# Performance work log

Hardware: AMD Instinct MI355X
Metric: run time of the kernel (lower is better)

The kernel has to match this reference:

```python
import jax, jax.numpy as jnp
import numpy as np

B, S, H, MID = 8, 2048, 256, 32


def get_rotary_matrix(s, d):
    # Faithful to llama-from-scratch get_rotary_matrix: theta = 10000**(-2*(i-1)/d)
    pos = jnp.arange(s, dtype=jnp.float32)
    i = jnp.arange(d // 2, dtype=jnp.float32)
    theta = 10000.0 ** (-2.0 * (i - 1.0) / d)
    ang = pos[:, None] * theta[None, :]            # [s, d/2]
    c, sn = jnp.cos(ang), jnp.sin(ang)
    ev = 2 * jnp.arange(d // 2)
    od = ev + 1
    R = jnp.zeros((s, d, d), jnp.float32)
    R = R.at[:, ev, ev].set(c).at[:, od, od].set(c)
    R = R.at[:, ev, od].set(-sn).at[:, od, ev].set(sn)
    return R


def setup_inputs() -> dict:
    key = jax.random.key(0)
    ks = jax.random.split(key, 7)
    sc = 0.02
    x = jax.random.normal(ks[0], (B, S, H), jnp.float32)
    # nn.Linear weights: l1.weight [mid, in], l2.weight [out, mid]; y = x @ W.T
    wq1 = jax.random.normal(ks[1], (MID, H), jnp.float32) * sc
    wq2 = jax.random.normal(ks[2], (H, MID), jnp.float32) * sc
    wk1 = jax.random.normal(ks[3], (MID, H), jnp.float32) * sc
    wk2 = jax.random.normal(ks[4], (H, MID), jnp.float32) * sc
    wv1 = jax.random.normal(ks[5], (MID, H), jnp.float32) * sc
    wv2 = jax.random.normal(ks[6], (H, MID), jnp.float32) * sc
    r = get_rotary_matrix(S, H)                    # [S, H, H] buffer
    return {"x": x, "r": r, "wq1": wq1, "wq2": wq2, "wk1": wk1,
            "wk2": wk2, "wv1": wv1, "wv2": wv2}


def reference(x, r, wq1, wq2, wk1, wk2, wv1, wv2):
    b, s, h = x.shape
    q = (x @ wq1.T) @ wq2.T                        # LoRA q: [b,s,h]
    k = (x @ wk1.T) @ wk2.T
    v = (x @ wv1.T) @ wv2.T
    # RoPE as dense per-position rotation matmul (bmm over seq dim)
    qr = jnp.einsum('bsh,shk->bsk', q, r[:s])
    kr = jnp.einsum('bsh,shk->bsk', k, r[:s])
    attn = jnp.einsum('bqh,bkh->bqk', qr, kr) * (h ** -0.5)   # [b,s,s]
    mask = jnp.tril(jnp.ones((s, s), bool))
    attn = jnp.where(mask, attn, -jnp.inf)
    attn = jax.nn.softmax(attn, axis=-1)
    out = attn @ v                                 # [b,s,h]
    return out
```

## Files before the change

kernel.cpp:

```cpp
#include <hip/hip_runtime.h>
#include <hip/hip_bf16.h>
#include <math.h>

typedef float f32x4 __attribute__((ext_vector_type(4)));
typedef float f32x16 __attribute__((ext_vector_type(16)));
typedef unsigned int u32x4 __attribute__((ext_vector_type(4)));
typedef __bf16 bf16x8 __attribute__((ext_vector_type(8)));
typedef unsigned short u16;

#define MFMA16(acc, a, b)                                              \
  acc = __builtin_amdgcn_mfma_f32_16x16x32_bf16(                       \
      __builtin_bit_cast(bf16x8, a), __builtin_bit_cast(bf16x8, b),    \
      acc, 0, 0, 0)

#define MFMA32(acc, a, b)                                              \
  acc = __builtin_amdgcn_mfma_f32_32x32x16_bf16(                       \
      __builtin_bit_cast(bf16x8, a), __builtin_bit_cast(bf16x8, b),    \
      acc, 0, 0, 0)

#define GLOAD_LDS16(gp, lp)                                            \
  __builtin_amdgcn_global_load_lds(                                    \
      (const __attribute__((address_space(1))) void*)(const void*)(gp),\
      (__attribute__((address_space(3))) void*)(void*)(lp), 16, 0, 0)

__device__ __forceinline__ u16 f2bf(float f) {
  union { float f; unsigned u; } v; v.f = f;
  unsigned r = v.u + 0x7FFFu + ((v.u >> 16) & 1u);
  return (u16)(r >> 16);
}

__device__ __forceinline__ float b2f(u16 h) {
  union { unsigned u; float f; } v; v.u = ((unsigned)h) << 16; return v.f;
}

__device__ __forceinline__ unsigned cvtpk(float lo, float hi) {
  unsigned r;
  asm("v_cvt_pk_bf16_f32 %0, %1, %2" : "=v"(r) : "v"(lo), "v"(hi));
  return r;
}

#define BFEX(vec, e) ((u16)(((e) & 1) ? ((vec)[(e) >> 1] >> 16) : ((vec)[(e) >> 1] & 0xffffu)))

__global__ __launch_bounds__(256) void proj_kernel(
    const float* __restrict__ x,
    const float* __restrict__ w1q, const float* __restrict__ w2q,
    const float* __restrict__ w1k, const float* __restrict__ w2k,
    const float* __restrict__ w1v, const float* __restrict__ w2v,
    u16* __restrict__ qout, u16* __restrict__ kout, u16* __restrict__ vout)
{
  __shared__ __align__(16) u16 smem[37376];
  u16* xs  = smem;
  u16* w1s = smem + 16384;
  u16* w2s = smem + 24576;
  u16* tls = smem + 34816;
  u16* bnc = smem;

  const int tid = threadIdx.x;
  const int w = tid >> 6, l = tid & 63;
  const int l15 = l & 15, lg = l >> 4;
  const int row0 = blockIdx.x * 64;
  const int p = blockIdx.y;

  const float* w1 = (p == 0) ? w1q : (p == 1) ? w1k : w1v;
  const float* w2 = (p == 0) ? w2q : (p == 1) ? w2k : w2v;
  u16* outp = (p == 0) ? qout : (p == 1) ? kout : vout;
  const bool dorope = (p < 2);

  #pragma unroll
  for (int i = 0; i < 16; ++i) {
    int idx = tid + 256 * i;
    int r = idx >> 6, c4 = idx & 63;
    float4 v = reinterpret_cast<const float4*>(x)[(size_t)(row0 + r) * 64 + c4];
    int ci = (c4 * 4) ^ ((r & 7) << 3);
    *reinterpret_cast<ushort4*>(&xs[r * 256 + ci]) =
        make_ushort4(f2bf(v.x), f2bf(v.y), f2bf(v.z), f2bf(v.w));
  }
  #pragma unroll
  for (int i = 0; i < 8; ++i) {
    int idx = tid + 256 * i;
    int r = idx >> 6, c4 = idx & 63;
    float4 v = reinterpret_cast<const float4*>(w1)[idx];
    int ci = (c4 * 4) ^ ((r & 7) << 3);
    *reinterpret_cast<ushort4*>(&w1s[r * 256 + ci]) =
        make_ushort4(f2bf(v.x), f2bf(v.y), f2bf(v.z), f2bf(v.w));
  }
  #pragma unroll
  for (int i = 0; i < 8; ++i) {
    int idx = tid + 256 * i;
    int r = idx >> 3, c4 = idx & 7;
    float4 v = reinterpret_cast<const float4*>(w2)[idx];
    *reinterpret_cast<ushort4*>(&w2s[r * 40 + c4 * 4]) =
        make_ushort4(f2bf(v.x), f2bf(v.y), f2bf(v.z), f2bf(v.w));
  }
  __syncthreads();

  f32x4 acc0 = {0.f, 0.f, 0.f, 0.f}, acc1 = {0.f, 0.f, 0.f, 0.f};
  {
    const int arow = w * 16 + l15;
    #pragma unroll
    for (int kk = 0; kk < 8; ++kk) {
      u32x4 a = *reinterpret_cast<const u32x4*>(
          &xs[arow * 256 + ((kk * 32 + lg * 8) ^ ((arow & 7) << 3))]);
      const int b0r = l15, b1r = l15 + 16;
      u32x4 b0 = *reinterpret_cast<const u32x4*>(
          &w1s[b0r * 256 + ((kk * 32 + lg * 8) ^ ((b0r & 7) << 3))]);
      u32x4 b1 = *reinterpret_cast<const u32x4*>(
          &w1s[b1r * 256 + ((kk * 32 + lg * 8) ^ ((b1r & 7) << 3))]);
      MFMA16(acc0, a, b0);
      MFMA16(acc1, a, b1);
    }
  }
  #pragma unroll
  for (int rr = 0; rr < 4; ++rr) {
    int trow = w * 16 + lg * 4 + rr;
    tls[trow * 40 + l15]      = f2bf(acc0[rr]);
    tls[trow * 40 + 16 + l15] = f2bf(acc1[rr]);
  }

  f32x4 yac[16];
  #pragma unroll
  for (int oc = 0; oc < 16; ++oc) yac[oc] = (f32x4){0.f, 0.f, 0.f, 0.f};
  {
    u32x4 a = *reinterpret_cast<const u32x4*>(&tls[(w * 16 + l15) * 40 + lg * 8]);
    #pragma unroll
    for (int oc = 0; oc < 16; ++oc) {
      u32x4 b = *reinterpret_cast<const u32x4*>(&w2s[(oc * 16 + l15) * 40 + lg * 8]);
      MFMA16(yac[oc], a, b);
    }
  }
  __syncthreads();

  #pragma unroll
  for (int oc = 0; oc < 16; ++oc)
    #pragma unroll
    for (int rr = 0; rr < 4; ++rr)
      bnc[(w * 16 + lg * 4 + rr) * 264 + oc * 16 + l15] = f2bf(yac[oc][rr]);
  __syncthreads();

  {
    const int frow = tid >> 2, c0 = (tid & 3) * 64;
    const int grow = row0 + frow;
    const int sidx = grow & 2047;
    const float sfl = (float)sidx;
    #pragma unroll
    for (int seg = 0; seg < 8; ++seg) {
      u32x4 v8 = *reinterpret_cast<const u32x4*>(&bnc[frow * 264 + c0 + seg * 8]);
      u32x4 res = v8;
      if (dorope) {
        #pragma unroll
        for (int j = 0; j < 4; ++j) {
          int jp = (c0 >> 1) + seg * 4 + j;
          float theta = __builtin_exp2f(13.287712379549449f *
                                        (2.f - 2.f * (float)jp) * (1.f / 256.f));
          float ang = sfl * theta;
          float sn, c;
          sincosf(ang, &sn, &c);
          float ev = b2f(BFEX(v8, 2 * j)), od = b2f(BFEX(v8, 2 * j + 1));
          u16 re = f2bf(ev * c + od * sn);
          u16 ro = f2bf(od * c - ev * sn);
          res[j] = ((unsigned)ro << 16) | (unsigned)re;
        }
      }
      *reinterpret_cast<u32x4*>(&outp[(size_t)grow * 256 + c0 + seg * 8]) = res;
    }
  }
}

__global__ __launch_bounds__(256, 2) void attn_kernel(
    const u16* __restrict__ qg, const u16* __restrict__ kg,
    const u16* __restrict__ vg, u16* __restrict__ po,
    float* __restrict__ pmw, float* __restrict__ plw)
{
  __shared__ __align__(16) u16 ks2[2][32 * 256];
  __shared__ __align__(16) u16 vt2[2][256 * 40];
  __shared__ float paxw[4][32];

  const int tid = threadIdx.x;
  const int w = tid >> 6, l = tid & 63;
  const int s = w >> 1, h2 = w & 1;
  const int q31 = l & 31, g = l >> 5;

  const int bx = blockIdx.x;
  const int bb = bx & 7;
  const int o_ = bx >> 3;
  const int idx = (o_ < 32) ? o_ : 95 - o_;
  const int qt = 31 - (idx >> 1);
  const int hv = idx & 1;
  const int tmx = 2 * qt + 1;

  const int qbase = qt * 64;
  const size_t boff = (size_t)bb * (2048 * 256);
  const int qg_ = qbase + s * 32 + q31;

  u32x4 qf[16];
  {
    const u16* qp = qg + boff + (size_t)qg_ * 256 + g * 8;
    #pragma unroll
    for (int st = 0; st < 16; ++st)
      qf[st] = *reinterpret_cast<const u32x4*>(qp + st * 16);
  }

  f32x16 o[4];
  #pragma unroll
  for (int dt = 0; dt < 4; ++dt)
    #pragma unroll
    for (int r = 0; r < 16; ++r) o[dt][r] = 0.f;
  float m_run = -INFINITY, l_run = 0.f;

  const int vc = tid & 31;
  const int kvr = (tid >> 5) * 4;
  const int swv = (vc & 3) << 3;
  const int swr = (q31 >> 3) << 3;
  const int ksw = (q31 & 7) << 3;
  const int kbase = q31 * 256;

  const u16* kgb = kg + boff;
  const u16* vgb = vg + boff;

  {
    const u16* kp = kgb + (size_t)(hv * 32) * 256;
    #pragma unroll
    for (int j = 0; j < 4; ++j) {
      int i2 = tid + 256 * j;
      int r = i2 >> 5, c8 = (i2 & 31) * 8;
      GLOAD_LDS16(kp + r * 256 + (c8 ^ ((r & 7) << 3)), &ks2[0][i2 * 8]);
    }
    const u16* vp = vgb + (size_t)(hv * 32) * 256;
    u32x4 vq[4];
    #pragma unroll
    for (int j = 0; j < 4; ++j)
      vq[j] = *reinterpret_cast<const u32x4*>(vp + (size_t)(kvr + j) * 256 + vc * 8);
    #pragma unroll
    for (int e = 0; e < 8; ++e) {
      int d = vc * 8 + e;
      *reinterpret_cast<ushort4*>(&vt2[0][d * 40 + (kvr ^ swv)]) =
          make_ushort4(BFEX(vq[0], e), BFEX(vq[1], e), BFEX(vq[2], e), BFEX(vq[3], e));
    }
  }
  __syncthreads();

  int cur = 0;
  for (int t = hv; t <= tmx; t += 2) {
    const int kv0 = t * 32;
    const int nb = cur ^ 1;
    const bool pf = (t + 2 <= tmx);

    u32x4 vq[4];
    if (pf) {
      const u16* kp = kgb + (size_t)((t + 2) * 32) * 256;
      #pragma unroll
      for (int j = 0; j < 4; ++j) {
        int i2 = tid + 256 * j;
        int r = i2 >> 5, c8 = (i2 & 31) * 8;
        GLOAD_LDS16(kp + r * 256 + (c8 ^ ((r & 7) << 3)), &ks2[nb][i2 * 8]);
      }
      const u16* vp = vgb + (size_t)((t + 2) * 32) * 256;
      #pragma unroll
      for (int j = 0; j < 4; ++j)
        vq[j] = *reinterpret_cast<const u32x4*>(vp + (size_t)(kvr + j) * 256 + vc * 8);
    }

    f32x16 sca, scb;
    #pragma unroll
    for (int r = 0; r < 16; ++r) { sca[r] = 0.f; scb[r] = 0.f; }
    #pragma unroll
    for (int st = 0; st < 8; ++st) {
      u32x4 a0 = *reinterpret_cast<const u32x4*>(
          &ks2[cur][kbase + ((st * 32 + g * 8) ^ ksw)]);
      u32x4 a1 = *reinterpret_cast<const u32x4*>(
          &ks2[cur][kbase + ((st * 32 + 16 + g * 8) ^ ksw)]);
      MFMA32(sca, a0, qf[2 * st]);
      MFMA32(scb, a1, qf[2 * st + 1]);
    }

    f32x16 sc;
    #pragma unroll
    for (int r = 0; r < 16; ++r) sc[r] = (sca[r] + scb[r]) * 0.0625f;
    if (kv0 + 31 > qbase + s * 32) {
      #pragma unroll
      for (int r = 0; r < 16; ++r) {
        int kvg = kv0 + (r & 3) + 8 * (r >> 2) + 4 * g;
        if (kvg > qg_) sc[r] = -INFINITY;
      }
    }
    float red[8];
    #pragma unroll
    for (int i = 0; i < 8; ++i) red[i] = fmaxf(sc[i], sc[i + 8]);
    #pragma unroll
    for (int i = 0; i < 4; ++i) red[i] = fmaxf(red[i], red[i + 4]);
    float mx = fmaxf(fmaxf(red[0], red[1]), fmaxf(red[2], red[3]));
    mx = fmaxf(mx, __shfl_xor(mx, 32, 64));
    float mnew = fmaxf(m_run, mx);
    float msafe = fmaxf(mnew, -1e30f);
    float alpha = __expf(m_run - msafe);
    m_run = mnew;
    #pragma unroll
    for (int r = 0; r < 16; ++r) sc[r] = __expf(sc[r] - msafe);
    #pragma unroll
    for (int i = 0; i < 8; ++i) red[i] = sc[i] + sc[i + 8];
    #pragma unroll
    for (int i = 0; i < 4; ++i) red[i] = red[i] + red[i + 4];
    float lh = (red[0] + red[1]) + (red[2] + red[3]);
    lh += __shfl_xor(lh, 32, 64);
    l_run = l_run * alpha + lh;

    unsigned wv[8], xw[8];
    #pragma unroll
    for (int j = 0; j < 8; ++j) wv[j] = cvtpk(sc[2 * j], sc[2 * j + 1]);
    #pragma unroll
    for (int j = 0; j < 8; ++j) xw[j] = __shfl_xor(wv[j], 32, 64);
    u32x4 pa0, pa1;
    pa0[0] = g ? xw[2] : wv[0]; pa0[1] = g ? xw[3] : wv[1];
    pa0[2] = g ? wv[2] : xw[0]; pa0[3] = g ? wv[3] : xw[1];
    pa1[0] = g ? xw[6] : wv[4]; pa1[1] = g ? xw[7] : wv[5];
    pa1[2] = g ? wv[6] : xw[4]; pa1[3] = g ? wv[7] : xw[5];

    if (!__all(alpha == 1.0f)) {
      if (l < 32) paxw[w][l] = alpha;
      f32x4 aR[4];
      #pragma unroll
      for (int i = 0; i < 4; ++i)
        aR[i] = *reinterpret_cast<const f32x4*>(&paxw[w][i * 8 + 4 * g]);
      #pragma unroll
      for (int dt = 0; dt < 4; ++dt)
        #pragma unroll
        for (int r = 0; r < 16; ++r) o[dt][r] *= aR[r >> 2][r & 3];
    }

    #pragma unroll
    for (int dt = 0; dt < 4; ++dt) {
      int rb = (h2 * 128 + dt * 32 + q31) * 40;
      u32x4 b0 = *reinterpret_cast<const u32x4*>(&vt2[cur][rb + ((g * 8) ^ swr)]);
      u32x4 b1 = *reinterpret_cast<const u32x4*>(&vt2[cur][rb + ((16 + g * 8) ^ swr)]);
      MFMA32(o[dt], pa0, b0);
      MFMA32(o[dt], pa1, b1);
    }

    if (pf) {
      #pragma unroll
      for (int e = 0; e < 8; ++e) {
        int d = vc * 8 + e;
        *reinterpret_cast<ushort4*>(&vt2[nb][d * 40 + (kvr ^ swv)]) =
            make_ushort4(BFEX(vq[0], e), BFEX(vq[1], e), BFEX(vq[2], e), BFEX(vq[3], e));
      }
    }
    __syncthreads();
    cur ^= 1;
  }

  const int pidx = (bb * 32 + qt) * 2 + hv;
  u16* op = po + (size_t)pidx * (64 * 256);
  #pragma unroll
  for (int dt = 0; dt < 4; ++dt) {
    #pragma unroll
    for (int r = 0; r < 16; ++r) {
      int row = s * 32 + (r & 3) + 8 * (r >> 2) + 4 * g;
      int col = h2 * 128 + dt * 32 + q31;
      op[(size_t)row * 256 + col] = f2bf(o[dt][r]);
    }
  }
  if (h2 == 0 && l < 32) {
    pmw[pidx * 64 + s * 32 + l] = m_run;
    plw[pidx * 64 + s * 32 + l] = l_run;
  }
}

__global__ __launch_bounds__(256) void combine_kernel(
    const u16* __restrict__ po, const float* __restrict__ pm,
    const float* __restrict__ plv, float* __restrict__ outg)
{
  int idx = blockIdx.x * 256 + threadIdx.x;
  int d8 = idx & 31;
  int row = idx >> 5;
  int bb = row >> 11, qrem = row & 2047;
  int qt = qrem >> 6, r64 = qrem & 63;
  int p0 = (bb * 32 + qt) * 2;

  float m0 = pm[p0 * 64 + r64], m1 = pm[(p0 + 1) * 64 + r64];
  float l0 = plv[p0 * 64 + r64], l1 = plv[(p0 + 1) * 64 + r64];
  float mm = fmaxf(m0, m1);
  float w0 = __expf(m0 - mm), w1 = __expf(m1 - mm);
  float inv = 1.f / (l0 * w0 + l1 * w1);

  u32x4 a0 = *reinterpret_cast<const u32x4*>(
      po + (size_t)p0 * (64 * 256) + (size_t)r64 * 256 + d8 * 8);
  u32x4 a1 = *reinterpret_cast<const u32x4*>(
      po + (size_t)(p0 + 1) * (64 * 256) + (size_t)r64 * 256 + d8 * 8);
  f32x4 r0, r1;
  #pragma unroll
  for (int e = 0; e < 4; ++e)
    r0[e] = (b2f(BFEX(a0, e)) * w0 + b2f(BFEX(a1, e)) * w1) * inv;
  #pragma unroll
  for (int e = 0; e < 4; ++e)
    r1[e] = (b2f(BFEX(a0, e + 4)) * w0 + b2f(BFEX(a1, e + 4)) * w1) * inv;
  float* op = outg + (size_t)row * 256 + d8 * 8;
  *reinterpret_cast<f32x4*>(op) = r0;
  *reinterpret_cast<f32x4*>(op + 4) = r1;
}

extern "C" void kernel_launch(void* const* d_in, const int* in_sizes, int n_in,
                              void* d_out, int out_size, void* d_ws, size_t ws_size,
                              hipStream_t stream) {
  const float* x   = (const float*)d_in[0];
  const float* wq1 = (const float*)d_in[2];
  const float* wq2 = (const float*)d_in[3];
  const float* wk1 = (const float*)d_in[4];
  const float* wk2 = (const float*)d_in[5];
  const float* wv1 = (const float*)d_in[6];
  const float* wv2 = (const float*)d_in[7];

  const size_t NTOK = (size_t)8 * 2048;
  u16* qw = (u16*)d_ws;
  u16* kw = qw + NTOK * 256;
  u16* vw = kw + NTOK * 256;
  u16* po = vw + NTOK * 256;
  float* pm  = (float*)(po + (size_t)512 * 64 * 256);
  float* plv = pm + 512 * 64;

  proj_kernel<<<dim3(256, 3), 256, 0, stream>>>(x, wq1, wq2, wk1, wk2, wv1, wv2,
                                                qw, kw, vw);
  attn_kernel<<<512, 256, 0, stream>>>(qw, kw, vw, po, pm, plv);
  combine_kernel<<<2048, 256, 0, stream>>>(po, pm, plv, (float*)d_out);
}
```

Measured before the change: 94.62 us.

## Load x and w1 straight into MFMA registers and shrink LDS footprint

The projection kernel no longer stages x and w1 through swizzled LDS. Each lane reads its fp32 fragments from global memory, packs them to bf16 with v_cvt_pk, and feeds them directly to the MFMA. The output bounce buffer is halved and the epilogue now runs in two passes, each covering 32 rows, to cut shared memory use and allow more blocks per CU. The cost is strided, less coalesced global reads of x and w1, redundant w1 loads across waves, and extra barriers.

Measured after the change: 99.87 us. +5.6%, slower.

```diff
diff --git a/kernel.cpp b/kernel.cpp
--- a/kernel.cpp
+++ b/kernel.cpp
@@ -36,6 +36,13 @@
 __device__ __forceinline__ unsigned cvtpk(float lo, float hi) {
   unsigned r;
   asm("v_cvt_pk_bf16_f32 %0, %1, %2" : "=v"(r) : "v"(lo), "v"(hi));
+  return r;
+}
+
+__device__ __forceinline__ u32x4 pack8(float4 a, float4 b) {
+  u32x4 r;
+  r[0] = cvtpk(a.x, a.y); r[1] = cvtpk(a.z, a.w);
+  r[2] = cvtpk(b.x, b.y); r[3] = cvtpk(b.z, b.w);
   return r;
 }
 
@@ -48,12 +55,9 @@
     const float* __restrict__ w1v, const float* __restrict__ w2v,
     u16* __restrict__ qout, u16* __restrict__ kout, u16* __restrict__ vout)
 {
-  __shared__ __align__(16) u16 smem[37376];
-  u16* xs  = smem;
-  u16* w1s = smem + 16384;
-  u16* w2s = smem + 24576;
-  u16* tls = smem + 34816;
-  u16* bnc = smem;
+  __shared__ __align__(16) u16 w2s[256 * 40];
+  __shared__ __align__(16) u16 tls[64 * 40];
+  __shared__ __align__(16) u16 bnc[32 * 264];
 
   const int tid = threadIdx.x;
   const int w = tid >> 6, l = tid & 63;
@@ -66,24 +70,6 @@
   u16* outp = (p == 0) ? qout : (p == 1) ? kout : vout;
   const bool dorope = (p < 2);
 
-  #pragma unroll
-  for (int i = 0; i < 16; ++i) {
-    int idx = tid + 256 * i;
-    int r = idx >> 6, c4 = idx & 63;
-    float4 v = reinterpret_cast<const float4*>(x)[(size_t)(row0 + r) * 64 + c4];
-    int ci = (c4 * 4) ^ ((r & 7) << 3);
-    *reinterpret_cast<ushort4*>(&xs[r * 256 + ci]) =
-        make_ushort4(f2bf(v.x), f2bf(v.y), f2bf(v.z), f2bf(v.w));
-  }
-  #pragma unroll
-  for (int i = 0; i < 8; ++i) {
-    int idx = tid + 256 * i;
-    int r = idx >> 6, c4 = idx & 63;
-    float4 v = reinterpret_cast<const float4*>(w1)[idx];
-    int ci = (c4 * 4) ^ ((r & 7) << 3);
-    *reinterpret_cast<ushort4*>(&w1s[r * 256 + ci]) =
-        make_ushort4(f2bf(v.x), f2bf(v.y), f2bf(v.z), f2bf(v.w));
-  }
   #pragma unroll
   for (int i = 0; i < 8; ++i) {
     int idx = tid + 256 * i;
@@ -96,16 +82,16 @@
 
   f32x4 acc0 = {0.f, 0.f, 0.f, 0.f}, acc1 = {0.f, 0.f, 0.f, 0.f};
   {
-    const int arow = w * 16 + l15;
+    const float4* xr  = reinterpret_cast<const float4*>(
+        x + (size_t)(row0 + w * 16 + l15) * 256);
+    const float4* w1r0 = reinterpret_cast<const float4*>(w1 + l15 * 256);
+    const float4* w1r1 = reinterpret_cast<const float4*>(w1 + (l15 + 16) * 256);
     #pragma unroll
     for (int kk = 0; kk < 8; ++kk) {
-      u32x4 a = *reinterpret_cast<const u32x4*>(
-          &xs[arow * 256 + ((kk * 32 + lg * 8) ^ ((arow & 7) << 3))]);
-      const int b0r = l15, b1r = l15 + 16;
-      u32x4 b0 = *reinterpret_cast<const u32x4*>(
-          &w1s[b0r * 256 + ((kk * 32 + lg * 8) ^ ((b0r & 7) << 3))]);
-      u32x4 b1 = *reinterpret_cast<const u32x4*>(
-          &w1s[b1r * 256 + ((kk * 32 + lg * 8) ^ ((b1r & 7) << 3))]);
+      int c4 = kk * 8 + lg * 2;
+      u32x4 a  = pack8(xr[c4], xr[c4 + 1]);
+      u32x4 b0 = pack8(w1r0[c4], w1r0[c4 + 1]);
+      u32x4 b1 = pack8(w1r1[c4], w1r1[c4 + 1]);
       MFMA16(acc0, a, b0);
       MFMA16(acc1, a, b1);
     }
@@ -128,23 +114,25 @@
       MFMA16(yac[oc], a, b);
     }
   }
-  __syncthreads();
-
-  #pragma unroll
-  for (int oc = 0; oc < 16; ++oc)
-    #pragma unroll
-    for (int rr = 0; rr < 4; ++rr)
-      bnc[(w * 16 + lg * 4 + rr) * 264 + oc * 16 + l15] = f2bf(yac[oc][rr]);
-  __syncthreads();
-
-  {
-    const int frow = tid >> 2, c0 = (tid & 3) * 64;
-    const int grow = row0 + frow;
-    const int sidx = grow & 2047;
-    const float sfl = (float)sidx;
-    #pragma unroll
-    for (int seg = 0; seg < 8; ++seg) {
-      u32x4 v8 = *reinterpret_cast<const u32x4*>(&bnc[frow * 264 + c0 + seg * 8]);
+
+  #pragma unroll
+  for (int half = 0; half < 2; ++half) {
+    __syncthreads();
+    if ((w >> 1) == half) {
+      const int wl = w & 1;
+      #pragma unroll
+      for (int oc = 0; oc < 16; ++oc)
+        #pragma unroll
+        for (int rr = 0; rr < 4; ++rr)
+          bnc[(wl * 16 + lg * 4 + rr) * 264 + oc * 16 + l15] = f2bf(yac[oc][rr]);
+    }
+    __syncthreads();
+    const int brow = tid >> 3, c0 = (tid & 7) * 32;
+    const int grow = row0 + half * 32 + brow;
+    const float sfl = (float)(grow & 2047);
+    #pragma unroll
+    for (int seg = 0; seg < 4; ++seg) {
+      u32x4 v8 = *reinterpret_cast<const u32x4*>(&bnc[brow * 264 + c0 + seg * 8]);
       u32x4 res = v8;
       if (dorope) {
         #pragma unroll
```

## Reuse x tile across q/k/v projections and swizzle V-transpose LDS rows

Applied to the files above, without the earlier changes.

The projection kernel now loads and converts each 32-row x tile once and loops over the three projections inside one block, instead of launching a separate block per projection that reloads x. The grid changes from 256x3 blocks of 64 rows to 512 blocks of 32 rows, with the low-rank stage run by only two waves and the second stage split across four waves. The attention kernel also XOR-swizzles the row index of the transposed V tile in LDS to reduce bank conflicts on the transpose writes and MFMA B-operand reads. Costs: weights are reloaded three times per block, there are more barriers, and two waves sit idle during the first matmul.

Result: slower. 105.9 us (+11.9%).

```diff
diff --git a/kernel.cpp b/kernel.cpp
--- a/kernel.cpp
+++ b/kernel.cpp
@@ -48,26 +48,19 @@
     const float* __restrict__ w1v, const float* __restrict__ w2v,
     u16* __restrict__ qout, u16* __restrict__ kout, u16* __restrict__ vout)
 {
-  __shared__ __align__(16) u16 smem[37376];
-  u16* xs  = smem;
-  u16* w1s = smem + 16384;
-  u16* w2s = smem + 24576;
-  u16* tls = smem + 34816;
-  u16* bnc = smem;
+  __shared__ __align__(16) u16 xs[32 * 256];
+  __shared__ __align__(16) u16 w1s[32 * 256];
+  __shared__ __align__(16) u16 w2s[256 * 40];
+  __shared__ __align__(16) u16 tls[32 * 40];
+  __shared__ __align__(16) u16 bnc[32 * 264];
 
   const int tid = threadIdx.x;
   const int w = tid >> 6, l = tid & 63;
   const int l15 = l & 15, lg = l >> 4;
-  const int row0 = blockIdx.x * 64;
-  const int p = blockIdx.y;
-
-  const float* w1 = (p == 0) ? w1q : (p == 1) ? w1k : w1v;
-  const float* w2 = (p == 0) ? w2q : (p == 1) ? w2k : w2v;
-  u16* outp = (p == 0) ? qout : (p == 1) ? kout : vout;
-  const bool dorope = (p < 2);
+  const int row0 = blockIdx.x * 32;
 
   #pragma unroll
-  for (int i = 0; i < 16; ++i) {
+  for (int i = 0; i < 8; ++i) {
     int idx = tid + 256 * i;
     int r = idx >> 6, c4 = idx & 63;
     float4 v = reinterpret_cast<const float4*>(x)[(size_t)(row0 + r) * 64 + c4];
@@ -75,93 +68,105 @@
     *reinterpret_cast<ushort4*>(&xs[r * 256 + ci]) =
         make_ushort4(f2bf(v.x), f2bf(v.y), f2bf(v.z), f2bf(v.w));
   }
-  #pragma unroll
-  for (int i = 0; i < 8; ++i) {
-    int idx = tid + 256 * i;
-    int r = idx >> 6, c4 = idx & 63;
-    float4 v = reinterpret_cast<const float4*>(w1)[idx];
-    int ci = (c4 * 4) ^ ((r & 7) << 3);
-    *reinterpret_cast<ushort4*>(&w1s[r * 256 + ci]) =
-        make_ushort4(f2bf(v.x), f2bf(v.y), f2bf(v.z), f2bf(v.w));
-  }
-  #pragma unroll
-  for (int i = 0; i < 8; ++i) {
-    int idx = tid + 256 * i;
-    int r = idx >> 3, c4 = idx & 7;
-    float4 v = reinterpret_cast<const float4*>(w2)[idx];
-    *reinterpret_cast<ushort4*>(&w2s[r * 40 + c4 * 4]) =
-        make_ushort4(f2bf(v.x), f2bf(v.y), f2bf(v.z), f2bf(v.w));
-  }
-  __syncthreads();
-
-  f32x4 acc0 = {0.f, 0.f, 0.f, 0.f}, acc1 = {0.f, 0.f, 0.f, 0.f};
-  {
-    const int arow = w * 16 + l15;
-    #pragma unroll
-    for (int kk = 0; kk < 8; ++kk) {
-      u32x4 a = *reinterpret_cast<const u32x4*>(
-          &xs[arow * 256 + ((kk * 32 + lg * 8) ^ ((arow & 7) << 3))]);
-      const int b0r = l15, b1r = l15 + 16;
-      u32x4 b0 = *reinterpret_cast<const u32x4*>(
-          &w1s[b0r * 256 + ((kk * 32 + lg * 8) ^ ((b0r & 7) << 3))]);
-      u32x4 b1 = *reinterpret_cast<const u32x4*>(
-          &w1s[b1r * 256 + ((kk * 32 + lg * 8) ^ ((b1r & 7) << 3))]);
-      MFMA16(acc0, a, b0);
-      MFMA16(acc1, a, b1);
-    }
-  }
-  #pragma unroll
-  for (int rr = 0; rr < 4; ++rr) {
-    int trow = w * 16 + lg * 4 + rr;
-    tls[trow * 40 + l15]      = f2bf(acc0[rr]);
-    tls[trow * 40 + 16 + l15] = f2bf(acc1[rr]);
-  }
-
-  f32x4 yac[16];
-  #pragma unroll
-  for (int oc = 0; oc < 16; ++oc) yac[oc] = (f32x4){0.f, 0.f, 0.f, 0.f};
-  {
-    u32x4 a = *reinterpret_cast<const u32x4*>(&tls[(w * 16 + l15) * 40 + lg * 8]);
-    #pragma unroll
-    for (int oc = 0; oc < 16; ++oc) {
-      u32x4 b = *reinterpret_cast<const u32x4*>(&w2s[(oc * 16 + l15) * 40 + lg * 8]);
-      MFMA16(yac[oc], a, b);
-    }
-  }
-  __syncthreads();
-
-  #pragma unroll
-  for (int oc = 0; oc < 16; ++oc)
-    #pragma unroll
-    for (int rr = 0; rr < 4; ++rr)
-      bnc[(w * 16 + lg * 4 + rr) * 264 + oc * 16 + l15] = f2bf(yac[oc][rr]);
-  __syncthreads();
-
-  {
-    const int frow = tid >> 2, c0 = (tid & 3) * 64;
-    const int grow = row0 + frow;
-    const int sidx = grow & 2047;
-    const float sfl = (float)sidx;
-    #pragma unroll
-    for (int seg = 0; seg < 8; ++seg) {
-      u32x4 v8 = *reinterpret_cast<const u32x4*>(&bnc[frow * 264 + c0 + seg * 8]);
-      u32x4 res = v8;
-      if (dorope) {
-        #pragma unroll
-        for (int j = 0; j < 4; ++j) {
-          int jp = (c0 >> 1) + seg * 4 + j;
-          float theta = __builtin_exp2f(13.287712379549449f *
-                                        (2.f - 2.f * (float)jp) * (1.f / 256.f));
-          float ang = sfl * theta;
-          float sn, c;
-          sincosf(ang, &sn, &c);
-          float ev = b2f(BFEX(v8, 2 * j)), od = b2f(BFEX(v8, 2 * j + 1));
-          u16 re = f2bf(ev * c + od * sn);
-          u16 ro = f2bf(od * c - ev * sn);
-          res[j] = ((unsigned)ro << 16) | (unsigned)re;
+
+  const float* W1[3] = {w1q, w1k, w1v};
+  const float* W2[3] = {w2q, w2k, w2v};
+  u16* OUT[3] = {qout, kout, vout};
+
+  for (int p = 0; p < 3; ++p) {
+    __syncthreads();
+    const float* w1 = W1[p];
+    const float* w2 = W2[p];
+    #pragma unroll
+    for (int i = 0; i < 8; ++i) {
+      int idx = tid + 256 * i;
+      int r = idx >> 6, c4 = idx & 63;
+      float4 v = reinterpret_cast<const float4*>(w1)[idx];
+      int ci = (c4 * 4) ^ ((r & 7) << 3);
+      *reinterpret_cast<ushort4*>(&w1s[r * 256 + ci]) =
+          make_ushort4(f2bf(v.x), f2bf(v.y), f2bf(v.z), f2bf(v.w));
+    }
+    #pragma unroll
+    for (int i = 0; i < 8; ++i) {
+      int idx = tid + 256 * i;
+      int r = idx >> 3, c4 = idx & 7;
+      float4 v = reinterpret_cast<const float4*>(w2)[idx];
+      *reinterpret_cast<ushort4*>(&w2s[r * 40 + c4 * 4]) =
+          make_ushort4(f2bf(v.x), f2bf(v.y), f2bf(v.z), f2bf(v.w));
+    }
+    __syncthreads();
+
+    if (w < 2) {
+      f32x4 acc0 = {0.f, 0.f, 0.f, 0.f}, acc1 = {0.f, 0.f, 0.f, 0.f};
+      const int arow = w * 16 + l15;
+      #pragma unroll
+      for (int kk = 0; kk < 8; ++kk) {
+        u32x4 a = *reinterpret_cast<const u32x4*>(
+            &xs[arow * 256 + ((kk * 32 + lg * 8) ^ ((arow & 7) << 3))]);
+        const int b0r = l15, b1r = l15 + 16;
+        u32x4 b0 = *reinterpret_cast<const u32x4*>(
+            &w1s[b0r * 256 + ((kk * 32 + lg * 8) ^ ((b0r & 7) << 3))]);
+        u32x4 b1 = *reinterpret_cast<const u32x4*>(
+            &w1s[b1r * 256 + ((kk * 32 + lg * 8) ^ ((b1r & 7) << 3))]);
+        MFMA16(acc0, a, b0);
+        MFMA16(acc1, a, b1);
+      }
+      #pragma unroll
+      for (int rr = 0; rr < 4; ++rr) {
+        int trow = w * 16 + lg * 4 + rr;
+        tls[trow * 40 + l15]      = f2bf(acc0[rr]);
+        tls[trow * 40 + 16 + l15] = f2bf(acc1[rr]);
+      }
+    }
+    __syncthreads();
+
+    const int rt = w >> 1, oc8 = (w & 1) * 8;
+    f32x4 yac[8];
+    #pragma unroll
+    for (int j = 0; j < 8; ++j) yac[j] = (f32x4){0.f, 0.f, 0.f, 0.f};
+    {
+      u32x4 a = *reinterpret_cast<const u32x4*>(&tls[(rt * 16 + l15) * 40 + lg * 8]);
+      #pragma unroll
+      for (int j = 0; j < 8; ++j) {
+        int oc = oc8 + j;
+        u32x4 b = *reinterpret_cast<const u32x4*>(&w2s[(oc * 16 + l15) * 40 + lg * 8]);
+        MFMA16(yac[j], a, b);
+      }
+    }
+    #pragma unroll
+    for (int j = 0; j < 8; ++j)
+      #pragma unroll
+      for (int rr = 0; rr < 4; ++rr)
+        bnc[(rt * 16 + lg * 4 + rr) * 264 + (oc8 + j) * 16 + l15] = f2bf(yac[j][rr]);
+    __syncthreads();
+
+    {
+      const int brow = tid >> 3, c0 = (tid & 7) * 32;
+      const int grow = row0 + brow;
+      const float sfl = (float)(grow & 2047);
+      u16* outp = OUT[p];
+      const bool dorope = (p < 2);
+      #pragma unroll
+      for (int seg = 0; seg < 4; ++seg) {
+        u32x4 v8 = *reinterpret_cast<const u32x4*>(&bnc[brow * 264 + c0 + seg * 8]);
+        u32x4 res = v8;
+        if (dorope) {
+          #pragma unroll
+          for (int j = 0; j < 4; ++j) {
+            int jp = (c0 >> 1) + seg * 4 + j;
+            float theta = __builtin_exp2f(13.287712379549449f *
+                                          (2.f - 2.f * (float)jp) * (1.f / 256.f));
+            float ang = sfl * theta;
+            float sn, c;
+            sincosf(ang, &sn, &c);
+            float ev = b2f(BFEX(v8, 2 * j)), od = b2f(BFEX(v8, 2 * j + 1));
+            u16 re = f2bf(ev * c + od * sn);
+            u16 ro = f2bf(od * c - ev * sn);
+            res[j] = ((unsigned)ro << 16) | (unsigned)re;
+          }
         }
-      }
-      *reinterpret_cast<u32x4*>(&outp[(size_t)grow * 256 + c0 + seg * 8]) = res;
+        *reinterpret_cast<u32x4*>(&outp[(size_t)grow * 256 + c0 + seg * 8]) = res;
+      }
     }
   }
 }
@@ -232,8 +237,8 @@
       vq[j] = *reinterpret_cast<const u32x4*>(vp + (size_t)(kvr + j) * 256 + vc * 8);
     #pragma unroll
     for (int e = 0; e < 8; ++e) {
-      int d = vc * 8 + e;
-      *reinterpret_cast<ushort4*>(&vt2[0][d * 40 + (kvr ^ swv)]) =
+      int pd = (vc * 8 + e) ^ (vc & 7);
+      *reinterpret_cast<ushort4*>(&vt2[0][pd * 40 + (kvr ^ swv)]) =
           make_ushort4(BFEX(vq[0], e), BFEX(vq[1], e), BFEX(vq[2], e), BFEX(vq[3], e));
     }
   }
@@ -329,7 +334,8 @@
 
     #pragma unroll
     for (int dt = 0; dt < 4; ++dt) {
-      int rb = (h2 * 128 + dt * 32 + q31) * 40;
+      int d = h2 * 128 + dt * 32 + q31;
+      int rb = (d ^ ((d >> 3) & 7)) * 40;
       u32x4 b0 = *reinterpret_cast<const u32x4*>(&vt2[cur][rb + ((g * 8) ^ swr)]);
       u32x4 b1 = *reinterpret_cast<const u32x4*>(&vt2[cur][rb + ((16 + g * 8) ^ swr)]);
       MFMA32(o[dt], pa0, b0);
@@ -339,8 +345,8 @@
     if (pf) {
       #pragma unroll
       for (int e = 0; e < 8; ++e) {
-        int d = vc * 8 + e;
-        *reinterpret_cast<ushort4*>(&vt2[nb][d * 40 + (kvr ^ swv)]) =
+        int pd = (vc * 8 + e) ^ (vc & 7);
+        *reinterpret_cast<ushort4*>(&vt2[nb][pd * 40 + (kvr ^ swv)]) =
             make_ushort4(BFEX(vq[0], e), BFEX(vq[1], e), BFEX(vq[2], e), BFEX(vq[3], e));
       }
     }
@@ -417,8 +423,8 @@
   float* pm  = (float*)(po + (size_t)512 * 64 * 256);
   float* plv = pm + 512 * 64;
 
-  proj_kernel<<<dim3(256, 3), 256, 0, stream>>>(x, wq1, wq2, wk1, wk2, wv1, wv2,
-                                                qw, kw, vw);
+  proj_kernel<<<512, 256, 0, stream>>>(x, wq1, wq2, wk1, wk2, wv1, wv2,
+                                       qw, kw, vw);
   attn_kernel<<<512, 256, 0, stream>>>(qw, kw, vw, po, pm, plv);
   combine_kernel<<<2048, 256, 0, stream>>>(po, pm, plv, (float*)d_out);
 }
```
